# Optimization experiments

Measured on AMD Instinct MI355X. Metric: run time of the kernel, lower is better.

## Reference

```python
import jax, jax.numpy as jnp
import numpy as np

B = 65536          # batch
E = 512            # embedding_dim
SL = 128           # speed_latent_dim
H = 256            # hidden_size
NB = 6             # num_branch
D = E + SL         # 640, branch input dim


def _linear_init(k, din, dout):
    bound = 1.0 / np.sqrt(din)
    kw, kb = jax.random.split(k)
    W = jax.random.uniform(kw, (din, dout), minval=-bound, maxval=bound, dtype=jnp.float32)
    b = jax.random.uniform(kb, (dout,), minval=-bound, maxval=bound, dtype=jnp.float32)
    return W, b


def setup_inputs() -> dict:
    key = jax.random.key(0)
    ks = jax.random.split(key, 10)
    embedding = jax.random.normal(ks[0], (B, E), dtype=jnp.float32)
    speed = jax.random.uniform(ks[1], (B, 1), dtype=jnp.float32)
    command = jax.random.randint(ks[2], (B,), 1, NB + 1)  # values in 1..6

    # speed_in: Linear(1,H) -> ReLU -> Linear(H,SL)
    si_W1, si_b1 = _linear_init(ks[3], 1, H)
    si_W2, si_b2 = _linear_init(ks[4], H, SL)

    # speed_out: Linear(D,H) -> ReLU -> Linear(H,H) -> ReLU -> Linear(H,1)
    so_W1, so_b1 = _linear_init(ks[5], D, H)
    so_W2, so_b2 = _linear_init(ks[6], H, H)
    so_W3, so_b3 = _linear_init(ks[7], H, 1)

    # NB branches, each Linear(D,H)->ReLU->Linear(H,H)->ReLU->Linear(H,3)->Sigmoid
    def mk_branch(k):
        k1, k2, k3 = jax.random.split(k, 3)
        W1, b1 = _linear_init(k1, D, H)
        W2, b2 = _linear_init(k2, H, H)
        W3, b3 = _linear_init(k3, H, 3)
        return W1, b1, W2, b2, W3, b3

    bW1, bb1, bW2, bb2, bW3, bb3 = jax.vmap(mk_branch)(jax.random.split(ks[8], NB))

    return {
        "embedding": embedding, "speed": speed, "command": command,
        "si_W1": si_W1, "si_b1": si_b1, "si_W2": si_W2, "si_b2": si_b2,
        "bW1": bW1, "bb1": bb1, "bW2": bW2, "bb2": bb2, "bW3": bW3, "bb3": bb3,
        "so_W1": so_W1, "so_b1": so_b1, "so_W2": so_W2, "so_b2": so_b2,
        "so_W3": so_W3, "so_b3": so_b3,
    }


def reference(embedding, speed, command,
              si_W1, si_b1, si_W2, si_b2,
              bW1, bb1, bW2, bb2, bW3, bb3,
              so_W1, so_b1, so_W2, so_b2, so_W3, so_b3):
    # speed_in MLP and concat
    s = jax.nn.relu(speed @ si_W1 + si_b1) @ si_W2 + si_b2          # [B, SL]
    emb = jnp.concatenate([embedding, s], axis=1)                    # [B, D]

    # all branches computed densely (as in the torch module), then one-hot mask
    h1 = jax.nn.relu(jnp.einsum('bd,ndh->nbh', emb, bW1) + bb1[:, None, :])   # [NB,B,H]
    h2 = jax.nn.relu(jnp.einsum('nbh,nhk->nbk', h1, bW2) + bb2[:, None, :])   # [NB,B,H]
    out = jax.nn.sigmoid(jnp.einsum('nbk,nko->nbo', h2, bW3) + bb3[:, None, :])  # [NB,B,3]

    mask = (jnp.arange(NB)[:, None] == (command - 1)[None, :]).astype(out.dtype)  # [NB,B]
    control_pred = jnp.sum(out * mask[:, :, None], axis=0)           # [B, 3]

    # speed prediction head
    sp = jax.nn.relu(emb @ so_W1 + so_b1)
    sp = jax.nn.relu(sp @ so_W2 + so_b2)
    speed_pred = sp @ so_W3 + so_b3                                  # [B, 1]

    return control_pred, speed_pred
```

## Files before the change

### kernel.cpp

```cpp
#include <hip/hip_runtime.h>
#include <cstdint>
#include <cstddef>

typedef _Float16 f16;
typedef f16 f16x8 __attribute__((ext_vector_type(8)));
typedef float f32x4 __attribute__((ext_vector_type(4)));

#define B_ROWS 65536
#define NT_BRANCH 1030
#define NT_SPEED 1024

constexpr size_t OFF_SF16   = 0;
constexpr size_t SZ_SF16    = (size_t)B_ROWS * 128 * 2;
constexpr size_t OFF_SIW2T  = OFF_SF16 + SZ_SF16;
constexpr size_t SZ_SIW2T   = (size_t)128 * 256 * 2;
constexpr size_t OFF_BW1T   = OFF_SIW2T + SZ_SIW2T;
constexpr size_t SZ_BW1T    = (size_t)6 * 256 * 640 * 2;
constexpr size_t OFF_BW2T   = OFF_BW1T + SZ_BW1T;
constexpr size_t SZ_BW2T    = (size_t)6 * 256 * 256 * 2;
constexpr size_t OFF_SOW1T  = OFF_BW2T + SZ_BW2T;
constexpr size_t SZ_SOW1T   = (size_t)256 * 640 * 2;
constexpr size_t OFF_SOW2T  = OFF_SOW1T + SZ_SOW1T;
constexpr size_t SZ_SOW2T   = (size_t)256 * 256 * 2;
constexpr size_t OFF_BW3T16 = OFF_SOW2T + SZ_SOW2T;
constexpr size_t SZ_BW3T16  = (size_t)6 * 16 * 256 * 2;
constexpr size_t OFF_SOW3T16= OFF_BW3T16 + SZ_BW3T16;
constexpr size_t SZ_SOW3T16 = (size_t)16 * 256 * 2;
constexpr size_t OFF_COUNTS = OFF_SOW3T16 + SZ_SOW3T16;
constexpr size_t OFF_CURSORS= OFF_COUNTS + 256;
constexpr size_t OFF_BINBASE= OFF_CURSORS + 256;
constexpr size_t OFF_TILECMD= OFF_BINBASE + 256;
constexpr size_t OFF_PERM   = OFF_TILECMD + 4352;
constexpr size_t WS_NEEDED  = OFF_PERM + (size_t)NT_BRANCH * 64 * 4;

__global__ void prep_kernel(const float* __restrict__ siW2,
                            const float* __restrict__ bW1,
                            const float* __restrict__ bW2,
                            const float* __restrict__ soW1,
                            const float* __restrict__ soW2,
                            const float* __restrict__ bW3,
                            const float* __restrict__ soW3,
                            f16* __restrict__ siW2T, f16* __restrict__ bW1T,
                            f16* __restrict__ bW2T, f16* __restrict__ soW1T,
                            f16* __restrict__ soW2T,
                            f16* __restrict__ bW3T16, f16* __restrict__ soW3T16,
                            int* __restrict__ counts, int* __restrict__ cursors,
                            int* __restrict__ perm)
{
    const int bx = blockIdx.x;
    const int tx = threadIdx.x, ty = threadIdx.y;
    const int tid = ty * 32 + tx;
    if (bx >= 1601) {
        const int ib = bx - 1601;
        const int idx = ib * 256 + tid;
        if (idx < NT_BRANCH * 64) perm[idx] = -1;
        if (ib == 0 && tid < 6) { counts[tid] = 0; cursors[tid] = 0; }
        return;
    }
    if (bx == 1600) {
        for (int i = tid; i < 6 * 16 * 256; i += 256) {
            const int c = i >> 12, rem = i & 4095, n = rem >> 8, k = rem & 255;
            bW3T16[i] = (n < 3) ? (f16)bW3[((size_t)c * 256 + k) * 3 + n] : (f16)0;
        }
        for (int i = tid; i < 16 * 256; i += 256) {
            const int n = i >> 8, k = i & 255;
            soW3T16[i] = (n == 0) ? (f16)soW3[k] : (f16)0;
        }
        return;
    }
    const float* in; f16* out; int R, C, lb;
    if (bx < 960)       { int m = bx / 160;        lb = bx - m * 160;       in = bW1 + (size_t)m * 640 * 256; out = bW1T + (size_t)m * 640 * 256; R = 640; C = 256; }
    else if (bx < 1344) { int m = (bx - 960) / 64; lb = (bx - 960) - m * 64; in = bW2 + (size_t)m * 256 * 256; out = bW2T + (size_t)m * 256 * 256; R = 256; C = 256; }
    else if (bx < 1504) { lb = bx - 1344; in = soW1; out = soW1T; R = 640; C = 256; }
    else if (bx < 1568) { lb = bx - 1504; in = soW2; out = soW2T; R = 256; C = 256; }
    else                { lb = bx - 1568; in = siW2; out = siW2T; R = 256; C = 128; }
    const int txt = C >> 5;
    const int c0 = (lb % txt) << 5;
    const int r0 = (lb / txt) << 5;
    __shared__ float tile[32][33];
    #pragma unroll
    for (int i = 0; i < 4; ++i)
        tile[tx][ty + 8 * i] = in[(size_t)(r0 + ty + 8 * i) * C + c0 + tx];
    __syncthreads();
    #pragma unroll
    for (int i = 0; i < 4; ++i)
        out[(size_t)(c0 + ty + 8 * i) * R + r0 + tx] = (f16)tile[ty + 8 * i][tx];
}

__global__ __launch_bounds__(256) void speedin_kernel(
    const float* __restrict__ speed,
    const float* __restrict__ siW1, const float* __restrict__ sib1,
    const f16* __restrict__ siW2T, const float* __restrict__ sib2,
    const int* __restrict__ cmd,
    f16* __restrict__ sF16, int* __restrict__ counts)
{
    __shared__ f16 H[64 * 264];
    __shared__ float spd[64];
    __shared__ int h[6];
    const int tid = threadIdx.x;
    const int rb = blockIdx.x * 64;
    if (tid < 6) h[tid] = 0;
    __syncthreads();
    if (tid < 64) {
        spd[tid] = speed[rb + tid];
        atomicAdd(&h[cmd[rb + tid] - 1], 1);
    }
    __syncthreads();
    if (tid < 6 && h[tid] > 0) atomicAdd(&counts[tid], h[tid]);
    {
        const float w1 = siW1[tid], b1v = sib1[tid];
        #pragma unroll 4
        for (int r = 0; r < 64; ++r) {
            float hv = spd[r] * w1 + b1v;
            H[r * 264 + tid] = (f16)(hv > 0.f ? hv : 0.f);
        }
    }
    __syncthreads();
    const int w = tid >> 6, lane = tid & 63, lq = lane >> 4, l16 = lane & 15;
    const int nb = w * 32;
    f32x4 acc[4][2];
    #pragma unroll
    for (int mt = 0; mt < 4; ++mt)
        #pragma unroll
        for (int nt = 0; nt < 2; ++nt)
            acc[mt][nt] = (f32x4){0.f, 0.f, 0.f, 0.f};
    for (int ks = 0; ks < 8; ++ks) {
        const int koff = ks * 32 + lq * 8;
        f16x8 af[4], bf[2];
        #pragma unroll
        for (int mt = 0; mt < 4; ++mt)
            af[mt] = *(const f16x8*)(&H[(mt * 16 + l16) * 264 + koff]);
        #pragma unroll
        for (int nt = 0; nt < 2; ++nt)
            bf[nt] = *(const f16x8*)(siW2T + (size_t)(nb + nt * 16 + l16) * 256 + koff);
        #pragma unroll
        for (int mt = 0; mt < 4; ++mt)
            #pragma unroll
            for (int nt = 0; nt < 2; ++nt)
                acc[mt][nt] = __builtin_amdgcn_mfma_f32_16x16x32_f16(af[mt], bf[nt], acc[mt][nt], 0, 0, 0);
    }
    #pragma unroll
    for (int mt = 0; mt < 4; ++mt)
        #pragma unroll
        for (int nt = 0; nt < 2; ++nt) {
            const int n = nb + nt * 16 + l16;
            const float bv = sib2[n];
            #pragma unroll
            for (int r2 = 0; r2 < 4; ++r2) {
                const int m = mt * 16 + lq * 4 + r2;
                sF16[(size_t)(rb + m) * 128 + n] = (f16)(acc[mt][nt][r2] + bv);
            }
        }
}

__global__ void plan_kernel(const int* __restrict__ counts,
                            int* __restrict__ binBase, int* __restrict__ tile_cmd) {
    __shared__ int tbase[7];
    if (threadIdx.x == 0) {
        int base = 0, tb = 0;
        for (int c = 0; c < 6; ++c) {
            binBase[c] = base;
            tbase[c] = tb;
            const int nt = (counts[c] + 63) >> 6;
            tb += nt;
            base += nt << 6;
        }
        tbase[6] = tb;
    }
    __syncthreads();
    for (int t = threadIdx.x; t < NT_BRANCH; t += 256) {
        int c = -1;
        #pragma unroll
        for (int j = 0; j < 6; ++j)
            if (t >= tbase[j] && t < tbase[j + 1]) c = j;
        tile_cmd[t] = c;
    }
}

__global__ void place_kernel(const int* __restrict__ cmd,
                             const int* __restrict__ binBase,
                             int* __restrict__ cursors, int* __restrict__ perm) {
    __shared__ int lcnt[6], lbase[6];
    const int tid = threadIdx.x;
    if (tid < 6) lcnt[tid] = 0;
    __syncthreads();
    const int i = blockIdx.x * 256 + tid;
    const int c = cmd[i] - 1;
    const int myr = atomicAdd(&lcnt[c], 1);
    __syncthreads();
    if (tid < 6) lbase[tid] = atomicAdd(&cursors[tid], lcnt[tid]);
    __syncthreads();
    perm[binBase[c] + lbase[c] + myr] = i;
}

__device__ __forceinline__ f16x8 stage_load(const float* __restrict__ srcF,
                                            const f16* __restrict__ srcH,
                                            int kc, int p) {
    if (kc < 8) {
        const float* s = srcF + kc * 64 + p * 8;
        const float4 f0 = ((const float4*)s)[0];
        const float4 f1 = ((const float4*)s)[1];
        f16x8 v;
        v[0] = (f16)f0.x; v[1] = (f16)f0.y; v[2] = (f16)f0.z; v[3] = (f16)f0.w;
        v[4] = (f16)f1.x; v[5] = (f16)f1.y; v[6] = (f16)f1.z; v[7] = (f16)f1.w;
        return v;
    } else {
        return *(const f16x8*)(srcH + (kc - 8) * 64 + p * 8);
    }
}

__global__ __launch_bounds__(512, 4) void heads_kernel(
    const float* __restrict__ emb,
    const f16* __restrict__ sF16,
    const int* __restrict__ perm, const int* __restrict__ tile_cmd,
    const f16* __restrict__ bW1T, const f16* __restrict__ bW2T,
    const f16* __restrict__ bW3T16,
    const float* __restrict__ bb1, const float* __restrict__ bb2,
    const float* __restrict__ bb3,
    const f16* __restrict__ soW1T, const f16* __restrict__ soW2T,
    const f16* __restrict__ soW3T16,
    const float* __restrict__ sob1, const float* __restrict__ sob2,
    const float* __restrict__ sob3,
    float* __restrict__ out)
{
    __shared__ f16 smem[16896];
    __shared__ int rowIdx[64];
    const int bx = blockIdx.x;
    const int tid = threadIdx.x;
    const bool is_speed = (bx >= NT_BRANCH);
    const f16 *W1T, *W2T, *W3T;
    const float *bias1, *bias2, *bias3;
    if (is_speed) {
        const int t = bx - NT_BRANCH;
        if (tid < 64) rowIdx[tid] = t * 64 + tid;
        W1T = soW1T; W2T = soW2T; W3T = soW3T16;
        bias1 = sob1; bias2 = sob2; bias3 = sob3;
    } else {
        const int c = tile_cmd[bx];
        if (c < 0) return;
        if (tid < 64) rowIdx[tid] = perm[bx * 64 + tid];
        W1T = bW1T + (size_t)c * 256 * 640;
        W2T = bW2T + (size_t)c * 256 * 256;
        W3T = bW3T16 + (size_t)c * 16 * 256;
        bias1 = bb1 + c * 256; bias2 = bb2 + c * 256; bias3 = bb3 + c * 3;
    }
    __syncthreads();

    const int r = tid >> 3, p = tid & 7;
    int growS = rowIdx[r]; if (growS < 0) growS = 0;
    const float* srcF = emb + (size_t)growS * 512;
    const f16*   srcH = sF16 + (size_t)growS * 128;
    const int pOff = r * 72 + p * 8;

    const int w = tid >> 6, lane = tid & 63, lq = lane >> 4, l16 = lane & 15;
    const int nb = w * 32;
    const f16* brow[2];
    #pragma unroll
    for (int nt = 0; nt < 2; ++nt)
        brow[nt] = W1T + (size_t)(nb + nt * 16 + l16) * 640;

    f32x4 acc[4][2];
    #pragma unroll
    for (int mt = 0; mt < 4; ++mt)
        #pragma unroll
        for (int nt = 0; nt < 2; ++nt)
            acc[mt][nt] = (f32x4){0.f, 0.f, 0.f, 0.f};

    f16x8 sreg[4];
    f16x8 Bb[2][2][2];
    #pragma unroll
    for (int j = 0; j < 4; ++j)
        sreg[j] = stage_load(srcF, srcH, j, p);
    #pragma unroll
    for (int ks = 0; ks < 2; ++ks)
        #pragma unroll
        for (int nt = 0; nt < 2; ++nt) {
            Bb[0][ks][nt] = *(const f16x8*)(brow[nt] + 0 * 64 + ks * 32 + lq * 8);
            Bb[1][ks][nt] = *(const f16x8*)(brow[nt] + 1 * 64 + ks * 32 + lq * 8);
        }
    *(f16x8*)(smem + pOff) = sreg[0];
    __syncthreads();
    #pragma unroll
    for (int kc = 0; kc < 10; ++kc) {
        f16* cur = smem + (kc & 1) * 4608;
        if (kc < 9)
            *(f16x8*)(smem + ((kc + 1) & 1) * 4608 + pOff) = sreg[(kc + 1) & 3];
        if (kc < 6)
            sreg[kc & 3] = stage_load(srcF, srcH, kc + 4, p);
        #pragma unroll
        for (int ks = 0; ks < 2; ++ks) {
            f16x8 a[4];
            #pragma unroll
            for (int mt = 0; mt < 4; ++mt)
                a[mt] = *(const f16x8*)(cur + (mt * 16 + l16) * 72 + ks * 32 + lq * 8);
            #pragma unroll
            for (int mt = 0; mt < 4; ++mt)
                #pragma unroll
                for (int nt = 0; nt < 2; ++nt)
                    acc[mt][nt] = __builtin_amdgcn_mfma_f32_16x16x32_f16(a[mt], Bb[kc & 1][ks][nt], acc[mt][nt], 0, 0, 0);
        }
        if (kc < 8) {
            #pragma unroll
            for (int ks = 0; ks < 2; ++ks)
                #pragma unroll
                for (int nt = 0; nt < 2; ++nt)
                    Bb[kc & 1][ks][nt] = *(const f16x8*)(brow[nt] + (kc + 2) * 64 + ks * 32 + lq * 8);
        }
        __syncthreads();
    }

    const f16* brow2[2];
    #pragma unroll
    for (int nt = 0; nt < 2; ++nt)
        brow2[nt] = W2T + (size_t)(nb + nt * 16 + l16) * 256;
    f16x8 Bd[2][2];
    #pragma unroll
    for (int nt = 0; nt < 2; ++nt)
        Bd[0][nt] = *(const f16x8*)(brow2[nt] + lq * 8);

    #pragma unroll
    for (int mt = 0; mt < 4; ++mt)
        #pragma unroll
        for (int nt = 0; nt < 2; ++nt) {
            const int n = nb + nt * 16 + l16;
            const float bv = bias1[n];
            #pragma unroll
            for (int r2 = 0; r2 < 4; ++r2) {
                const int m = mt * 16 + lq * 4 + r2;
                const float v = acc[mt][nt][r2] + bv;
                smem[m * 264 + n] = (f16)(v > 0.f ? v : 0.f);
            }
            acc[mt][nt] = (f32x4){0.f, 0.f, 0.f, 0.f};
        }
    __syncthreads();

    #pragma unroll
    for (int ks = 0; ks < 8; ++ks) {
        if (ks < 7) {
            #pragma unroll
            for (int nt = 0; nt < 2; ++nt)
                Bd[(ks + 1) & 1][nt] = *(const f16x8*)(brow2[nt] + (ks + 1) * 32 + lq * 8);
        }
        f16x8 a[4];
        #pragma unroll
        for (int mt = 0; mt < 4; ++mt)
            a[mt] = *(const f16x8*)(&smem[(mt * 16 + l16) * 264 + ks * 32 + lq * 8]);
        #pragma unroll
        for (int mt = 0; mt < 4; ++mt)
            #pragma unroll
            for (int nt = 0; nt < 2; ++nt)
                acc[mt][nt] = __builtin_amdgcn_mfma_f32_16x16x32_f16(a[mt], Bd[ks & 1][nt], acc[mt][nt], 0, 0, 0);
    }
    __syncthreads();
    #pragma unroll
    for (int mt = 0; mt < 4; ++mt)
        #pragma unroll
        for (int nt = 0; nt < 2; ++nt) {
            const int n = nb + nt * 16 + l16;
            const float bv = bias2[n];
            #pragma unroll
            for (int r2 = 0; r2 < 4; ++r2) {
                const int m = mt * 16 + lq * 4 + r2;
                const float v = acc[mt][nt][r2] + bv;
                smem[m * 264 + n] = (f16)(v > 0.f ? v : 0.f);
            }
        }
    __syncthreads();
    if (w < 4) {
        f32x4 acc3 = (f32x4){0.f, 0.f, 0.f, 0.f};
        const f16* w3row = W3T + (size_t)l16 * 256;
        #pragma unroll
        for (int ks = 0; ks < 8; ++ks) {
            const int koff = ks * 32 + lq * 8;
            const f16x8 af = *(const f16x8*)(&smem[(w * 16 + l16) * 264 + koff]);
            const f16x8 bf = *(const f16x8*)(w3row + koff);
            acc3 = __builtin_amdgcn_mfma_f32_16x16x32_f16(af, bf, acc3, 0, 0, 0);
        }
        const int orow = w * 16 + lq * 4;
        if (!is_speed) {
            if (l16 < 3) {
                const float b3 = bias3[l16];
                #pragma unroll
                for (int r2 = 0; r2 < 4; ++r2) {
                    const int g = rowIdx[orow + r2];
                    if (g >= 0)
                        out[(size_t)g * 3 + l16] = 1.f / (1.f + __expf(-(acc3[r2] + b3)));
                }
            }
        } else {
            if (l16 == 0) {
                const float b3 = bias3[0];
                #pragma unroll
                for (int r2 = 0; r2 < 4; ++r2)
                    out[(size_t)3 * B_ROWS + rowIdx[orow + r2]] = acc3[r2] + b3;
            }
        }
    }
}

extern "C" void kernel_launch(void* const* d_in, const int* in_sizes, int n_in,
                              void* d_out, int out_size, void* d_ws, size_t ws_size,
                              hipStream_t stream) {
    (void)in_sizes; (void)n_in; (void)out_size; (void)ws_size;
    const float* embedding = (const float*)d_in[0];
    const float* speed     = (const float*)d_in[1];
    const int*   command   = (const int*)d_in[2];
    const float* si_W1 = (const float*)d_in[3];
    const float* si_b1 = (const float*)d_in[4];
    const float* si_W2 = (const float*)d_in[5];
    const float* si_b2 = (const float*)d_in[6];
    const float* bW1   = (const float*)d_in[7];
    const float* bb1   = (const float*)d_in[8];
    const float* bW2   = (const float*)d_in[9];
    const float* bb2   = (const float*)d_in[10];
    const float* bW3   = (const float*)d_in[11];
    const float* bb3   = (const float*)d_in[12];
    const float* so_W1 = (const float*)d_in[13];
    const float* so_b1 = (const float*)d_in[14];
    const float* so_W2 = (const float*)d_in[15];
    const float* so_b2 = (const float*)d_in[16];
    const float* so_W3 = (const float*)d_in[17];
    const float* so_b3 = (const float*)d_in[18];
    float* out = (float*)d_out;

    char* ws = (char*)d_ws;
    f16* sF16   = (f16*)(ws + OFF_SF16);
    f16* siW2T  = (f16*)(ws + OFF_SIW2T);
    f16* bW1T   = (f16*)(ws + OFF_BW1T);
    f16* bW2T   = (f16*)(ws + OFF_BW2T);
    f16* soW1T  = (f16*)(ws + OFF_SOW1T);
    f16* soW2T  = (f16*)(ws + OFF_SOW2T);
    f16* bW3T16 = (f16*)(ws + OFF_BW3T16);
    f16* soW3T16= (f16*)(ws + OFF_SOW3T16);
    int* counts = (int*)(ws + OFF_COUNTS);
    int* cursors= (int*)(ws + OFF_CURSORS);
    int* binBase= (int*)(ws + OFF_BINBASE);
    int* tile_cmd = (int*)(ws + OFF_TILECMD);
    int* perm   = (int*)(ws + OFF_PERM);

    prep_kernel<<<1859, dim3(32, 8), 0, stream>>>(
        si_W2, bW1, bW2, so_W1, so_W2, bW3, so_W3,
        siW2T, bW1T, bW2T, soW1T, soW2T, bW3T16, soW3T16,
        counts, cursors, perm);
    speedin_kernel<<<1024, 256, 0, stream>>>(
        speed, si_W1, si_b1, siW2T, si_b2, command, sF16, counts);
    plan_kernel<<<1, 256, 0, stream>>>(counts, binBase, tile_cmd);
    place_kernel<<<256, 256, 0, stream>>>(command, binBase, cursors, perm);
    heads_kernel<<<NT_BRANCH + NT_SPEED, 512, 0, stream>>>(
        embedding, sF16, perm, tile_cmd,
        bW1T, bW2T, bW3T16, bb1, bb2, bb3,
        soW1T, soW2T, soW3T16, so_b1, so_b2, so_b3, out);
}
```

Measured before the change: 376.7 us.

## Fuse speed head into branch tiles to share staged embedding loads

The separate speed-head tiles are removed, and each branch tile now also computes the speed head on its own permuted rows. The staged embedding/speed-latent A-operand is loaded from global memory once and reused for both weight sets, which removes a second full pass over the 64K×640 input. Shared memory doubles to hold both hidden activations, register pressure roughly doubles from the two accumulator sets, and the barrier is replaced by an inline-asm waitcnt+s_barrier. Occupancy may drop under the 512-thread, 4-block launch bound.

```diff
diff --git a/kernel.cpp b/kernel.cpp
--- a/kernel.cpp
+++ b/kernel.cpp
@@ -8,7 +8,6 @@
 
 #define B_ROWS 65536
 #define NT_BRANCH 1030
-#define NT_SPEED 1024
 
 constexpr size_t OFF_SF16   = 0;
 constexpr size_t SZ_SF16    = (size_t)B_ROWS * 128 * 2;
@@ -32,6 +31,9 @@
 constexpr size_t OFF_TILECMD= OFF_BINBASE + 256;
 constexpr size_t OFF_PERM   = OFF_TILECMD + 4352;
 constexpr size_t WS_NEEDED  = OFF_PERM + (size_t)NT_BRANCH * 64 * 4;
+
+#define MFMA16(a, b, c) __builtin_amdgcn_mfma_f32_16x16x32_f16(a, b, c, 0, 0, 0)
+#define BARSYNC() asm volatile("s_waitcnt lgkmcnt(0)\n\ts_barrier" ::: "memory")
 
 __global__ void prep_kernel(const float* __restrict__ siW2,
                             const float* __restrict__ bW1,
@@ -137,7 +139,7 @@
         for (int mt = 0; mt < 4; ++mt)
             #pragma unroll
             for (int nt = 0; nt < 2; ++nt)
-                acc[mt][nt] = __builtin_amdgcn_mfma_f32_16x16x32_f16(af[mt], bf[nt], acc[mt][nt], 0, 0, 0);
+                acc[mt][nt] = MFMA16(af[mt], bf[nt], acc[mt][nt]);
     }
     #pragma unroll
     for (int mt = 0; mt < 4; ++mt)
@@ -223,27 +225,19 @@
     const float* __restrict__ sob3,
     float* __restrict__ out)
 {
-    __shared__ f16 smem[16896];
+    __shared__ f16 smem[33792];
     __shared__ int rowIdx[64];
     const int bx = blockIdx.x;
     const int tid = threadIdx.x;
-    const bool is_speed = (bx >= NT_BRANCH);
-    const f16 *W1T, *W2T, *W3T;
-    const float *bias1, *bias2, *bias3;
-    if (is_speed) {
-        const int t = bx - NT_BRANCH;
-        if (tid < 64) rowIdx[tid] = t * 64 + tid;
-        W1T = soW1T; W2T = soW2T; W3T = soW3T16;
-        bias1 = sob1; bias2 = sob2; bias3 = sob3;
-    } else {
-        const int c = tile_cmd[bx];
-        if (c < 0) return;
-        if (tid < 64) rowIdx[tid] = perm[bx * 64 + tid];
-        W1T = bW1T + (size_t)c * 256 * 640;
-        W2T = bW2T + (size_t)c * 256 * 256;
-        W3T = bW3T16 + (size_t)c * 16 * 256;
-        bias1 = bb1 + c * 256; bias2 = bb2 + c * 256; bias3 = bb3 + c * 3;
-    }
+    const int c = tile_cmd[bx];
+    if (c < 0) return;
+    if (tid < 64) rowIdx[tid] = perm[bx * 64 + tid];
+    const f16* __restrict__ W1b = bW1T + (size_t)c * 256 * 640;
+    const f16* __restrict__ W2b = bW2T + (size_t)c * 256 * 256;
+    const f16* __restrict__ W3b = bW3T16 + (size_t)c * 16 * 256;
+    const float* __restrict__ b1b = bb1 + c * 256;
+    const float* __restrict__ b2b = bb2 + c * 256;
+    const float* __restrict__ b3b = bb3 + c * 3;
     __syncthreads();
 
     const int r = tid >> 3, p = tid & 7;
@@ -254,132 +248,157 @@
 
     const int w = tid >> 6, lane = tid & 63, lq = lane >> 4, l16 = lane & 15;
     const int nb = w * 32;
-    const f16* brow[2];
-    #pragma unroll
-    for (int nt = 0; nt < 2; ++nt)
-        brow[nt] = W1T + (size_t)(nb + nt * 16 + l16) * 640;
-
-    f32x4 acc[4][2];
+    const int ro0 = (nb + l16) * 640;
+    const int ro1 = (nb + 16 + l16) * 640;
+
+    f32x4 aB[4][2], aS[4][2];
     #pragma unroll
     for (int mt = 0; mt < 4; ++mt)
         #pragma unroll
-        for (int nt = 0; nt < 2; ++nt)
-            acc[mt][nt] = (f32x4){0.f, 0.f, 0.f, 0.f};
+        for (int nt = 0; nt < 2; ++nt) {
+            aB[mt][nt] = (f32x4){0.f, 0.f, 0.f, 0.f};
+            aS[mt][nt] = (f32x4){0.f, 0.f, 0.f, 0.f};
+        }
 
     f16x8 sreg[4];
-    f16x8 Bb[2][2][2];
     #pragma unroll
     for (int j = 0; j < 4; ++j)
         sreg[j] = stage_load(srcF, srcH, j, p);
-    #pragma unroll
-    for (int ks = 0; ks < 2; ++ks)
-        #pragma unroll
-        for (int nt = 0; nt < 2; ++nt) {
-            Bb[0][ks][nt] = *(const f16x8*)(brow[nt] + 0 * 64 + ks * 32 + lq * 8);
-            Bb[1][ks][nt] = *(const f16x8*)(brow[nt] + 1 * 64 + ks * 32 + lq * 8);
-        }
+    f16x8 Bb[2], Bs[2];
+    Bb[0] = *(const f16x8*)(W1b + ro0 + lq * 8);
+    Bb[1] = *(const f16x8*)(W1b + ro1 + lq * 8);
+    Bs[0] = *(const f16x8*)(soW1T + ro0 + lq * 8);
+    Bs[1] = *(const f16x8*)(soW1T + ro1 + lq * 8);
     *(f16x8*)(smem + pOff) = sreg[0];
-    __syncthreads();
+    BARSYNC();
+
     #pragma unroll
     for (int kc = 0; kc < 10; ++kc) {
-        f16* cur = smem + (kc & 1) * 4608;
+        const f16* cur = smem + (kc & 1) * 4608;
         if (kc < 9)
             *(f16x8*)(smem + ((kc + 1) & 1) * 4608 + pOff) = sreg[(kc + 1) & 3];
         if (kc < 6)
             sreg[kc & 3] = stage_load(srcF, srcH, kc + 4, p);
-        #pragma unroll
-        for (int ks = 0; ks < 2; ++ks) {
-            f16x8 a[4];
-            #pragma unroll
-            for (int mt = 0; mt < 4; ++mt)
-                a[mt] = *(const f16x8*)(cur + (mt * 16 + l16) * 72 + ks * 32 + lq * 8);
-            #pragma unroll
-            for (int mt = 0; mt < 4; ++mt)
-                #pragma unroll
-                for (int nt = 0; nt < 2; ++nt)
-                    acc[mt][nt] = __builtin_amdgcn_mfma_f32_16x16x32_f16(a[mt], Bb[kc & 1][ks][nt], acc[mt][nt], 0, 0, 0);
-        }
-        if (kc < 8) {
-            #pragma unroll
-            for (int ks = 0; ks < 2; ++ks)
-                #pragma unroll
-                for (int nt = 0; nt < 2; ++nt)
-                    Bb[kc & 1][ks][nt] = *(const f16x8*)(brow[nt] + (kc + 2) * 64 + ks * 32 + lq * 8);
-        }
-        __syncthreads();
-    }
-
-    const f16* brow2[2];
-    #pragma unroll
-    for (int nt = 0; nt < 2; ++nt)
-        brow2[nt] = W2T + (size_t)(nb + nt * 16 + l16) * 256;
-    f16x8 Bd[2][2];
-    #pragma unroll
-    for (int nt = 0; nt < 2; ++nt)
-        Bd[0][nt] = *(const f16x8*)(brow2[nt] + lq * 8);
+        f16x8 a0[4];
+        #pragma unroll
+        for (int mt = 0; mt < 4; ++mt)
+            a0[mt] = *(const f16x8*)(cur + (mt * 16 + l16) * 72 + lq * 8);
+        f16x8 B1b[2], B1s[2];
+        B1b[0] = *(const f16x8*)(W1b + ro0 + kc * 64 + 32 + lq * 8);
+        B1b[1] = *(const f16x8*)(W1b + ro1 + kc * 64 + 32 + lq * 8);
+        B1s[0] = *(const f16x8*)(soW1T + ro0 + kc * 64 + 32 + lq * 8);
+        B1s[1] = *(const f16x8*)(soW1T + ro1 + kc * 64 + 32 + lq * 8);
+        #pragma unroll
+        for (int mt = 0; mt < 4; ++mt) {
+            aB[mt][0] = MFMA16(a0[mt], Bb[0], aB[mt][0]);
+            aB[mt][1] = MFMA16(a0[mt], Bb[1], aB[mt][1]);
+            aS[mt][0] = MFMA16(a0[mt], Bs[0], aS[mt][0]);
+            aS[mt][1] = MFMA16(a0[mt], Bs[1], aS[mt][1]);
+        }
+        if (kc < 9) {
+            Bb[0] = *(const f16x8*)(W1b + ro0 + (kc + 1) * 64 + lq * 8);
+            Bb[1] = *(const f16x8*)(W1b + ro1 + (kc + 1) * 64 + lq * 8);
+            Bs[0] = *(const f16x8*)(soW1T + ro0 + (kc + 1) * 64 + lq * 8);
+            Bs[1] = *(const f16x8*)(soW1T + ro1 + (kc + 1) * 64 + lq * 8);
+        }
+        f16x8 a1[4];
+        #pragma unroll
+        for (int mt = 0; mt < 4; ++mt)
+            a1[mt] = *(const f16x8*)(cur + (mt * 16 + l16) * 72 + 32 + lq * 8);
+        #pragma unroll
+        for (int mt = 0; mt < 4; ++mt) {
+            aB[mt][0] = MFMA16(a1[mt], B1b[0], aB[mt][0]);
+            aB[mt][1] = MFMA16(a1[mt], B1b[1], aB[mt][1]);
+            aS[mt][0] = MFMA16(a1[mt], B1s[0], aS[mt][0]);
+            aS[mt][1] = MFMA16(a1[mt], B1s[1], aS[mt][1]);
+        }
+        BARSYNC();
+    }
+
+    const int r2o0 = (nb + l16) * 256;
+    const int r2o1 = (nb + 16 + l16) * 256;
+    f16x8 Cb[2][2], Cs[2][2];
+    Cb[0][0] = *(const f16x8*)(W2b + r2o0 + lq * 8);
+    Cb[0][1] = *(const f16x8*)(W2b + r2o1 + lq * 8);
+    Cs[0][0] = *(const f16x8*)(soW2T + r2o0 + lq * 8);
+    Cs[0][1] = *(const f16x8*)(soW2T + r2o1 + lq * 8);
 
     #pragma unroll
     for (int mt = 0; mt < 4; ++mt)
         #pragma unroll
         for (int nt = 0; nt < 2; ++nt) {
             const int n = nb + nt * 16 + l16;
-            const float bv = bias1[n];
+            const float fB = b1b[n], fS = sob1[n];
             #pragma unroll
             for (int r2 = 0; r2 < 4; ++r2) {
                 const int m = mt * 16 + lq * 4 + r2;
-                const float v = acc[mt][nt][r2] + bv;
-                smem[m * 264 + n] = (f16)(v > 0.f ? v : 0.f);
+                const float vB = aB[mt][nt][r2] + fB;
+                const float vS = aS[mt][nt][r2] + fS;
+                smem[m * 264 + n] = (f16)(vB > 0.f ? vB : 0.f);
+                smem[16896 + m * 264 + n] = (f16)(vS > 0.f ? vS : 0.f);
             }
-            acc[mt][nt] = (f32x4){0.f, 0.f, 0.f, 0.f};
-        }
-    __syncthreads();
+            aB[mt][nt] = (f32x4){0.f, 0.f, 0.f, 0.f};
+            aS[mt][nt] = (f32x4){0.f, 0.f, 0.f, 0.f};
+        }
+    BARSYNC();
 
     #pragma unroll
     for (int ks = 0; ks < 8; ++ks) {
         if (ks < 7) {
-            #pragma unroll
-            for (int nt = 0; nt < 2; ++nt)
-                Bd[(ks + 1) & 1][nt] = *(const f16x8*)(brow2[nt] + (ks + 1) * 32 + lq * 8);
-        }
-        f16x8 a[4];
-        #pragma unroll
-        for (int mt = 0; mt < 4; ++mt)
-            a[mt] = *(const f16x8*)(&smem[(mt * 16 + l16) * 264 + ks * 32 + lq * 8]);
-        #pragma unroll
-        for (int mt = 0; mt < 4; ++mt)
-            #pragma unroll
-            for (int nt = 0; nt < 2; ++nt)
-                acc[mt][nt] = __builtin_amdgcn_mfma_f32_16x16x32_f16(a[mt], Bd[ks & 1][nt], acc[mt][nt], 0, 0, 0);
-    }
-    __syncthreads();
+            Cb[(ks + 1) & 1][0] = *(const f16x8*)(W2b + r2o0 + (ks + 1) * 32 + lq * 8);
+            Cb[(ks + 1) & 1][1] = *(const f16x8*)(W2b + r2o1 + (ks + 1) * 32 + lq * 8);
+            Cs[(ks + 1) & 1][0] = *(const f16x8*)(soW2T + r2o0 + (ks + 1) * 32 + lq * 8);
+            Cs[(ks + 1) & 1][1] = *(const f16x8*)(soW2T + r2o1 + (ks + 1) * 32 + lq * 8);
+        }
+        f16x8 ab[4], as2[4];
+        #pragma unroll
+        for (int mt = 0; mt < 4; ++mt) {
+            ab[mt]  = *(const f16x8*)(&smem[(mt * 16 + l16) * 264 + ks * 32 + lq * 8]);
+            as2[mt] = *(const f16x8*)(&smem[16896 + (mt * 16 + l16) * 264 + ks * 32 + lq * 8]);
+        }
+        #pragma unroll
+        for (int mt = 0; mt < 4; ++mt) {
+            aB[mt][0] = MFMA16(ab[mt],  Cb[ks & 1][0], aB[mt][0]);
+            aB[mt][1] = MFMA16(ab[mt],  Cb[ks & 1][1], aB[mt][1]);
+            aS[mt][0] = MFMA16(as2[mt], Cs[ks & 1][0], aS[mt][0]);
+            aS[mt][1] = MFMA16(as2[mt], Cs[ks & 1][1], aS[mt][1]);
+        }
+    }
+    BARSYNC();
+
     #pragma unroll
     for (int mt = 0; mt < 4; ++mt)
         #pragma unroll
         for (int nt = 0; nt < 2; ++nt) {
             const int n = nb + nt * 16 + l16;
-            const float bv = bias2[n];
+            const float fB = b2b[n], fS = sob2[n];
             #pragma unroll
             for (int r2 = 0; r2 < 4; ++r2) {
                 const int m = mt * 16 + lq * 4 + r2;
-                const float v = acc[mt][nt][r2] + bv;
-                smem[m * 264 + n] = (f16)(v > 0.f ? v : 0.f);
+                const float vB = aB[mt][nt][r2] + fB;
+                const float vS = aS[mt][nt][r2] + fS;
+                smem[m * 264 + n] = (f16)(vB > 0.f ? vB : 0.f);
+                smem[16896 + m * 264 + n] = (f16)(vS > 0.f ? vS : 0.f);
             }
         }
-    __syncthreads();
-    if (w < 4) {
+    BARSYNC();
+
+    {
         f32x4 acc3 = (f32x4){0.f, 0.f, 0.f, 0.f};
-        const f16* w3row = W3T + (size_t)l16 * 256;
+        const int hb = (w < 4) ? 0 : 16896;
+        const int wrow = (w & 3) * 16;
+        const f16* w3row = ((w < 4) ? W3b : soW3T16) + (size_t)l16 * 256;
         #pragma unroll
         for (int ks = 0; ks < 8; ++ks) {
             const int koff = ks * 32 + lq * 8;
-            const f16x8 af = *(const f16x8*)(&smem[(w * 16 + l16) * 264 + koff]);
+            const f16x8 af = *(const f16x8*)(&smem[hb + (wrow + l16) * 264 + koff]);
             const f16x8 bf = *(const f16x8*)(w3row + koff);
-            acc3 = __builtin_amdgcn_mfma_f32_16x16x32_f16(af, bf, acc3, 0, 0, 0);
-        }
-        const int orow = w * 16 + lq * 4;
-        if (!is_speed) {
+            acc3 = MFMA16(af, bf, acc3);
+        }
+        const int orow = wrow + lq * 4;
+        if (w < 4) {
             if (l16 < 3) {
-                const float b3 = bias3[l16];
+                const float b3 = b3b[l16];
                 #pragma unroll
                 for (int r2 = 0; r2 < 4; ++r2) {
                     const int g = rowIdx[orow + r2];
@@ -389,10 +408,13 @@
             }
         } else {
             if (l16 == 0) {
-                const float b3 = bias3[0];
+                const float b3 = sob3[0];
                 #pragma unroll
-                for (int r2 = 0; r2 < 4; ++r2)
-                    out[(size_t)3 * B_ROWS + rowIdx[orow + r2]] = acc3[r2] + b3;
+                for (int r2 = 0; r2 < 4; ++r2) {
+                    const int g = rowIdx[orow + r2];
+                    if (g >= 0)
+                        out[(size_t)3 * B_ROWS + g] = acc3[r2] + b3;
+                }
             }
         }
     }
@@ -446,7 +468,7 @@
         speed, si_W1, si_b1, siW2T, si_b2, command, sF16, counts);
     plan_kernel<<<1, 256, 0, stream>>>(counts, binBase, tile_cmd);
     place_kernel<<<256, 256, 0, stream>>>(command, binBase, cursors, perm);
-    heads_kernel<<<NT_BRANCH + NT_SPEED, 512, 0, stream>>>(
+    heads_kernel<<<NT_BRANCH, 512, 0, stream>>>(
         embedding, sF16, perm, tile_cmd,
         bW1T, bW2T, bW3T16, bb1, bb2, bb3,
         soW1T, soW2T, soW3T16, so_b1, so_b2, so_b3, out);
```

Result: slower. 501.0 us (+33.0%).
